# Kernel optimization log

Measured on AMD Instinct MI355X. Metric: run time of the kernel, lower is better.

Reference implementation:

```python
import jax, jax.numpy as jnp
import numpy as np

N_NODES = 50000
N_EDGES = 800000
VOCAB = 500
IN_DIM = 128
HID = 128
OUT_DIM = 64
N_GRAPHS = 512


def setup_inputs() -> dict:
    key = jax.random.key(0)
    ks = jax.random.split(key, 12)
    s = 0.05
    return {
        "emb": jax.random.normal(ks[0], (VOCAB, IN_DIM), jnp.float32) * s,
        "w1a": jax.random.normal(ks[1], (HID, IN_DIM), jnp.float32) * s,
        "b1a": jnp.zeros((HID,), jnp.float32),
        "w1b": jax.random.normal(ks[2], (HID, HID), jnp.float32) * s,
        "b1b": jnp.zeros((HID,), jnp.float32),
        "w2a": jax.random.normal(ks[3], (HID, HID), jnp.float32) * s,
        "b2a": jnp.zeros((HID,), jnp.float32),
        "w2b": jax.random.normal(ks[4], (HID, HID), jnp.float32) * s,
        "b2b": jnp.zeros((HID,), jnp.float32),
        "fc_w": jax.random.normal(ks[5], (OUT_DIM, HID), jnp.float32) * s,
        "fc_b": jnp.zeros((OUT_DIM,), jnp.float32),
        "x_idx": jax.random.randint(ks[6], (N_NODES,), 0, VOCAB, jnp.int32),
        "edge_index": jax.random.randint(ks[7], (2, N_EDGES), 0, N_NODES, jnp.int32),
        "batch": jnp.sort(jax.random.randint(ks[8], (N_NODES,), 0, N_GRAPHS, jnp.int32)),
    }


def gin_conv(x, wa, ba, wb, bb, src, dst):
    # GINConv with eps=0: MLP(x + sum_{j->i} x_j)
    agg = jax.ops.segment_sum(x[src], dst, num_segments=N_NODES)  # [N, d]
    h = x + agg
    h = jax.nn.relu(h @ wa.T + ba)
    return h @ wb.T + bb


def reference(emb, w1a, b1a, w1b, b1b, w2a, b2a, w2b, b2b, fc_w, fc_b,
              x_idx, edge_index, batch):
    src, dst = edge_index[0], edge_index[1]
    x = emb[x_idx]  # [N, IN_DIM] embedding lookup
    x = jax.nn.relu(gin_conv(x, w1a, b1a, w1b, b1b, src, dst))
    x = jax.nn.relu(gin_conv(x, w2a, b2a, w2b, b2b, src, dst))
    # global mean pool over graphs
    sums = jax.ops.segment_sum(x, batch, num_segments=N_GRAPHS)  # [G, HID]
    cnt = jax.ops.segment_sum(jnp.ones((N_NODES,), x.dtype), batch, num_segments=N_GRAPHS)
    pooled = sums / jnp.maximum(cnt, 1.0)[:, None]
    return pooled @ fc_w.T + fc_b  # [G, OUT_DIM]
```

## Files before the change

### kernel.cpp

```cpp
#include <hip/hip_runtime.h>

#define N_NODES 50000
#define N_EDGES 800000
#define DIM 128
#define NGRAPH 512
#define ODIM 64
#define VOCAB 500
#define NBKT 391
#define NB2 128
#define EPB2 (N_EDGES / NB2)
#define CAP 4096

typedef __attribute__((ext_vector_type(8))) short bf16x8;
typedef __attribute__((ext_vector_type(4))) short bf16x4;
typedef __attribute__((ext_vector_type(4))) float f32x4;

__device__ inline unsigned short f2bf(float f) {
  unsigned u = __builtin_bit_cast(unsigned, f);
  return (unsigned short)((u + 0x7fffu + ((u >> 16) & 1u)) >> 16);
}
__device__ inline float bf2f(unsigned short h) {
  unsigned u = ((unsigned)h) << 16;
  return __builtin_bit_cast(float, u);
}

__global__ __launch_bounds__(256) void prep_kernel(
    const float* __restrict__ emb,
    const float* __restrict__ w1a, const float* __restrict__ w1b,
    const float* __restrict__ w2a, const float* __restrict__ w2b,
    unsigned short* __restrict__ embb, unsigned short* __restrict__ wbf) {
  int u = blockIdx.x * 256 + threadIdx.x;
  const float* src;
  unsigned short* dst;
  if (u < VOCAB * 16) {
    src = emb + (size_t)u * 8;
    dst = embb + (size_t)u * 8;
  } else {
    int v = u - VOCAB * 16;
    if (v >= 4 * 2048) return;
    int m = v >> 11, loc = v & 2047;
    const float* w = (m == 0) ? w1a : (m == 1) ? w1b : (m == 2) ? w2a : w2b;
    src = w + (size_t)loc * 8;
    dst = wbf + (size_t)v * 8;
  }
  f32x4 a = ((const f32x4*)src)[0], b = ((const f32x4*)src)[1];
  bf16x8 o;
  #pragma unroll
  for (int e = 0; e < 4; ++e) {
    o[e] = (short)f2bf(a[e]);
    o[4 + e] = (short)f2bf(b[e]);
  }
  *(bf16x8*)dst = o;
}

__global__ __launch_bounds__(512) void bkt_hist_kernel(
    const int* __restrict__ ei, unsigned* __restrict__ HB) {
  __shared__ unsigned cnt[NBKT];
  int t = threadIdx.x, b = blockIdx.x;
  for (int i = t; i < NBKT; i += 512) cnt[i] = 0;
  __syncthreads();
  int base = b * EPB2;
  for (int i = t; i < EPB2; i += 512)
    atomicAdd(&cnt[(unsigned)ei[N_EDGES + base + i] >> 7], 1u);
  __syncthreads();
  for (int i = t; i < NBKT; i += 512) HB[(size_t)b * NBKT + i] = cnt[i];
}

__global__ __launch_bounds__(512) void bkt_scatter_kernel(
    const int* __restrict__ ei, const unsigned* __restrict__ HB,
    unsigned* __restrict__ eb, int* __restrict__ bktbase) {
  __shared__ unsigned cur[NBKT];
  __shared__ unsigned wsum[8];
  int t = threadIdx.x, b = blockIdx.x;
  int lane = t & 63, wid = t >> 6;
  unsigned pre = 0, tot = 0;
  if (t < NBKT) {
    for (int bb = 0; bb < NB2; ++bb) {
      unsigned h = HB[(size_t)bb * NBKT + t];
      pre += (bb < b) ? h : 0u;
      tot += h;
    }
  }
  unsigned s = tot;
  #pragma unroll
  for (int d = 1; d < 64; d <<= 1) {
    unsigned u = __shfl_up(s, d, 64);
    if (lane >= d) s += u;
  }
  if (lane == 63) wsum[wid] = s;
  __syncthreads();
  if (wid == 0) {
    unsigned ws = (lane < 8) ? wsum[lane] : 0u;
    #pragma unroll
    for (int d = 1; d < 8; d <<= 1) {
      unsigned u = __shfl_up(ws, d, 64);
      if (lane >= d) ws += u;
    }
    if (lane < 8) wsum[lane] = ws;
  }
  __syncthreads();
  unsigned base = s - tot + (wid ? wsum[wid - 1] : 0u);
  if (t < NBKT) cur[t] = base + pre;
  if (b == 0) {
    if (t < NBKT) bktbase[t] = (int)base;
    if (t == NBKT - 1) bktbase[NBKT] = (int)(base + tot);
  }
  __syncthreads();
  int ebase = b * EPB2;
  for (int i = t; i < EPB2; i += 512) {
    int sn = ei[ebase + i];
    unsigned d = (unsigned)ei[N_EDGES + ebase + i];
    unsigned pos = atomicAdd(&cur[d >> 7], 1u);
    eb[pos] = ((d & 127u) << 16) | (unsigned)sn;
  }
}

__global__ __launch_bounds__(512) void sort_bucket_kernel(
    const unsigned* __restrict__ eb, const int* __restrict__ bktbase,
    int* __restrict__ srt, int* __restrict__ row) {
  __shared__ unsigned stage[CAP];
  __shared__ unsigned short sorted[CAP];
  __shared__ unsigned hist[128], cur[128];
  __shared__ unsigned wtot;
  int t = threadIdx.x, bkt = blockIdx.x;
  int bs = bktbase[bkt], be = bktbase[bkt + 1];
  int cnt = be - bs;
  if (cnt > CAP) cnt = CAP;
  if (t < 128) hist[t] = 0;
  if (bkt == 0 && t == 0) row[N_NODES] = N_EDGES;
  __syncthreads();
  for (int i = t; i < cnt; i += 512) {
    unsigned e = eb[bs + i];
    stage[i] = e;
    atomicAdd(&hist[e >> 16], 1u);
  }
  __syncthreads();
  if (t < 128) {
    int lane = t & 63;
    unsigned v = hist[t], ss = v;
    #pragma unroll
    for (int d = 1; d < 64; d <<= 1) {
      unsigned u = __shfl_up(ss, d, 64);
      if (lane >= d) ss += u;
    }
    if (t == 63) wtot = ss;
    cur[t] = ss - v;
  }
  __syncthreads();
  if (t < 128) {
    unsigned e0 = cur[t] + (t >= 64 ? wtot : 0u);
    cur[t] = e0;
    int n = bkt * 128 + t;
    if (n < N_NODES) row[n] = bs + (int)e0;
  }
  __syncthreads();
  for (int i = t; i < cnt; i += 512) {
    unsigned e = stage[i];
    unsigned r = atomicAdd(&cur[e >> 16], 1u);
    sorted[r] = (unsigned short)(e & 0xFFFFu);
  }
  __syncthreads();
  for (int i = t; i < cnt; i += 512) srt[bs + i] = (int)sorted[i];
}

__global__ __launch_bounds__(256) void agg_emb_kernel(
    const unsigned short* __restrict__ embb, const int* __restrict__ xidx,
    const int* __restrict__ row, const int* __restrict__ srt,
    unsigned short* __restrict__ xa) {
  int n = blockIdx.x * 16 + (threadIdx.x >> 4);
  int c = threadIdx.x & 15;
  int lo = row[n], hi = row[n + 1];
  bf16x8 sv = *(const bf16x8*)(embb + (size_t)xidx[n] * DIM + c * 8);
  float a[8];
  #pragma unroll
  for (int e = 0; e < 8; ++e) a[e] = bf2f((unsigned short)sv[e]);
  int k = lo;
  for (; k + 8 <= hi; k += 8) {
    bf16x8 w[8];
    #pragma unroll
    for (int q = 0; q < 8; ++q)
      w[q] = *(const bf16x8*)(embb + (size_t)xidx[srt[k + q]] * DIM + c * 8);
    #pragma unroll
    for (int q = 0; q < 8; ++q)
      #pragma unroll
      for (int e = 0; e < 8; ++e) a[e] += bf2f((unsigned short)w[q][e]);
  }
  for (; k + 2 <= hi; k += 2) {
    bf16x8 w0 = *(const bf16x8*)(embb + (size_t)xidx[srt[k]] * DIM + c * 8);
    bf16x8 w1 = *(const bf16x8*)(embb + (size_t)xidx[srt[k + 1]] * DIM + c * 8);
    #pragma unroll
    for (int e = 0; e < 8; ++e)
      a[e] += bf2f((unsigned short)w0[e]) + bf2f((unsigned short)w1[e]);
  }
  if (k < hi) {
    bf16x8 w = *(const bf16x8*)(embb + (size_t)xidx[srt[k]] * DIM + c * 8);
    #pragma unroll
    for (int e = 0; e < 8; ++e) a[e] += bf2f((unsigned short)w[e]);
  }
  bf16x8 o;
  #pragma unroll
  for (int e = 0; e < 8; ++e) o[e] = (short)f2bf(a[e]);
  *(bf16x8*)(xa + (size_t)n * DIM + c * 8) = o;
}

__global__ __launch_bounds__(256) void agg_x_kernel(
    const unsigned short* __restrict__ x, const int* __restrict__ row,
    const int* __restrict__ srt, unsigned short* __restrict__ xa) {
  int n = blockIdx.x * 16 + (threadIdx.x >> 4);
  int c = threadIdx.x & 15;
  int lo = row[n], hi = row[n + 1];
  bf16x8 sv = *(const bf16x8*)(x + (size_t)n * DIM + c * 8);
  float a[8];
  #pragma unroll
  for (int e = 0; e < 8; ++e) a[e] = bf2f((unsigned short)sv[e]);
  int k = lo;
  for (; k + 8 <= hi; k += 8) {
    bf16x8 w[8];
    #pragma unroll
    for (int q = 0; q < 8; ++q)
      w[q] = *(const bf16x8*)(x + (size_t)srt[k + q] * DIM + c * 8);
    #pragma unroll
    for (int q = 0; q < 8; ++q)
      #pragma unroll
      for (int e = 0; e < 8; ++e) a[e] += bf2f((unsigned short)w[q][e]);
  }
  for (; k + 2 <= hi; k += 2) {
    bf16x8 w0 = *(const bf16x8*)(x + (size_t)srt[k] * DIM + c * 8);
    bf16x8 w1 = *(const bf16x8*)(x + (size_t)srt[k + 1] * DIM + c * 8);
    #pragma unroll
    for (int e = 0; e < 8; ++e)
      a[e] += bf2f((unsigned short)w0[e]) + bf2f((unsigned short)w1[e]);
  }
  if (k < hi) {
    bf16x8 w = *(const bf16x8*)(x + (size_t)srt[k] * DIM + c * 8);
    #pragma unroll
    for (int e = 0; e < 8; ++e) a[e] += bf2f((unsigned short)w[e]);
  }
  bf16x8 o;
  #pragma unroll
  for (int e = 0; e < 8; ++e) o[e] = (short)f2bf(a[e]);
  *(bf16x8*)(xa + (size_t)n * DIM + c * 8) = o;
}

__global__ __launch_bounds__(256) void mlp_mfma_kernel(
    const unsigned short* __restrict__ xa,
    const unsigned short* __restrict__ wabf, const float* __restrict__ ba,
    const unsigned short* __restrict__ wbbf, const float* __restrict__ bb,
    unsigned short* __restrict__ xout) {
  __shared__ short Xs[64 * 128];
  __shared__ short Hs[64 * 128];
  int t = threadIdx.x;
  int lane = t & 63;
  int w = t >> 6;
  int jq = w * 32;
  int l15 = lane & 15;
  int lg = lane >> 4;

  bf16x8 waf[2][4], wbf[2][4];
  #pragma unroll
  for (int jm = 0; jm < 2; ++jm) {
    int jrow = jq + jm * 16 + l15;
    #pragma unroll
    for (int ks = 0; ks < 4; ++ks) {
      int k0 = ks * 32 + lg * 8;
      waf[jm][ks] = *(const bf16x8*)(wabf + (size_t)jrow * DIM + k0);
      wbf[jm][ks] = *(const bf16x8*)(wbbf + (size_t)jrow * DIM + k0);
    }
  }
  f32x4 ba_r[2], bb_r[2];
  #pragma unroll
  for (int jm = 0; jm < 2; ++jm) {
    ba_r[jm] = *(const f32x4*)(ba + jq + jm * 16 + lg * 4);
    bb_r[jm] = *(const f32x4*)(bb + jq + jm * 16 + lg * 4);
  }

  for (int half = 0; half < 2; ++half) {
    int nbase = blockIdx.x * 128 + half * 64;

    {
      int r = t >> 2;
      int cb = (t & 3) * 4;
      int node = nbase + r;
      #pragma unroll
      for (int i = 0; i < 4; ++i) {
        int chunk = cb + i;
        bf16x8 v = {0, 0, 0, 0, 0, 0, 0, 0};
        if (node < N_NODES)
          v = *(const bf16x8*)(xa + (size_t)node * DIM + chunk * 8);
        *(bf16x8*)&Xs[r * 128 + ((chunk ^ (r & 7)) << 3)] = v;
      }
    }
    __syncthreads();

    #pragma unroll
    for (int nt = 0; nt < 4; ++nt) {
      int rrow = nt * 16 + l15;
      bf16x8 xf[4];
      #pragma unroll
      for (int ks = 0; ks < 4; ++ks) {
        int chunk = ks * 4 + lg;
        xf[ks] = *(const bf16x8*)&Xs[rrow * 128 + ((chunk ^ (rrow & 7)) << 3)];
      }
      #pragma unroll
      for (int jm = 0; jm < 2; ++jm) {
        f32x4 acc = ba_r[jm];
        #pragma unroll
        for (int ks = 0; ks < 4; ++ks)
          acc = __builtin_amdgcn_mfma_f32_16x16x32_bf16(waf[jm][ks], xf[ks], acc, 0, 0, 0);
        int hnode = nt * 16 + l15;
        int cbase = jq + jm * 16 + lg * 4;
        unsigned p0 = (unsigned)f2bf(fmaxf(acc[0], 0.f)) |
                      ((unsigned)f2bf(fmaxf(acc[1], 0.f)) << 16);
        unsigned p1 = (unsigned)f2bf(fmaxf(acc[2], 0.f)) |
                      ((unsigned)f2bf(fmaxf(acc[3], 0.f)) << 16);
        unsigned idx = hnode * 128 + (((cbase >> 3) ^ (hnode & 7)) << 3) + (cbase & 7);
        *(uint2*)&Hs[idx] = make_uint2(p0, p1);
      }
    }
    __syncthreads();

    #pragma unroll
    for (int nt = 0; nt < 4; ++nt) {
      int rrow = nt * 16 + l15;
      bf16x8 hf[4];
      #pragma unroll
      for (int ks = 0; ks < 4; ++ks) {
        int chunk = ks * 4 + lg;
        hf[ks] = *(const bf16x8*)&Hs[rrow * 128 + ((chunk ^ (rrow & 7)) << 3)];
      }
      #pragma unroll
      for (int jm = 0; jm < 2; ++jm) {
        f32x4 acc = bb_r[jm];
        #pragma unroll
        for (int ks = 0; ks < 4; ++ks)
          acc = __builtin_amdgcn_mfma_f32_16x16x32_bf16(wbf[jm][ks], hf[ks], acc, 0, 0, 0);
        int node = nbase + nt * 16 + l15;
        if (node < N_NODES) {
          bf16x4 o;
          #pragma unroll
          for (int e = 0; e < 4; ++e) o[e] = (short)f2bf(fmaxf(acc[e], 0.f));
          *(bf16x4*)(xout + (size_t)node * DIM + jq + jm * 16 + lg * 4) = o;
        }
      }
    }
    __syncthreads();
  }
}

#define PP 132
__global__ __launch_bounds__(256) void pool_fc_kernel(
    const unsigned short* __restrict__ x, const int* __restrict__ batch,
    const float* __restrict__ fcw, const float* __restrict__ fcb,
    float* __restrict__ out) {
  int g = blockIdx.x, t = threadIdx.x;
  __shared__ float part[16 * PP];
  __shared__ float pooled[DIM];
  __shared__ int sbound[2];
  if (t < 2) {
    int target = g + t;
    int lo = 0, hi = N_NODES;
    while (lo < hi) {
      int m = (lo + hi) >> 1;
      if (batch[m] < target) lo = m + 1; else hi = m;
    }
    sbound[t] = lo;
  }
  __syncthreads();
  int lo = sbound[0], hi = sbound[1];
  int r = t >> 4, c = t & 15;
  float acc[8] = {0.f, 0.f, 0.f, 0.f, 0.f, 0.f, 0.f, 0.f};
  for (int nn = lo + r; nn < hi; nn += 16) {
    bf16x8 v = *(const bf16x8*)(x + (size_t)nn * DIM + c * 8);
    #pragma unroll
    for (int e = 0; e < 8; ++e) acc[e] += bf2f((unsigned short)v[e]);
  }
  #pragma unroll
  for (int e = 0; e < 8; ++e) part[r * PP + c * 8 + e] = acc[e];
  __syncthreads();
  if (t < DIM) {
    float s = 0.f;
    #pragma unroll
    for (int rr = 0; rr < 16; ++rr) s += part[rr * PP + t];
    pooled[t] = s / fmaxf((float)(hi - lo), 1.0f);
  }
  __syncthreads();
  if (t < ODIM) {
    float a = fcb[t];
    const float* wr = fcw + (size_t)t * DIM;
    #pragma unroll 8
    for (int h = 0; h < DIM; ++h) a += pooled[h] * wr[h];
    out[(size_t)g * ODIM + t] = a;
  }
}

extern "C" void kernel_launch(void* const* d_in, const int* in_sizes, int n_in,
                              void* d_out, int out_size, void* d_ws, size_t ws_size,
                              hipStream_t stream) {
  const float* emb  = (const float*)d_in[0];
  const float* w1a  = (const float*)d_in[1];
  const float* b1a  = (const float*)d_in[2];
  const float* w1b  = (const float*)d_in[3];
  const float* b1b  = (const float*)d_in[4];
  const float* w2a  = (const float*)d_in[5];
  const float* b2a  = (const float*)d_in[6];
  const float* w2b  = (const float*)d_in[7];
  const float* b2b  = (const float*)d_in[8];
  const float* fcw  = (const float*)d_in[9];
  const float* fcb  = (const float*)d_in[10];
  const int*   xidx = (const int*)d_in[11];
  const int*   ei   = (const int*)d_in[12];
  const int*   batch= (const int*)d_in[13];
  float* out = (float*)d_out;

  size_t featb = (size_t)N_NODES * DIM * sizeof(unsigned short);
  char* ws = (char*)d_ws;
  unsigned short* B1 = (unsigned short*)ws;
  unsigned short* B2 = (unsigned short*)(ws + featb);
  char* p = ws + 2 * featb;
  unsigned short* embb = (unsigned short*)p;  p += (VOCAB * DIM * 2 + 15) / 16 * 16;
  unsigned short* wbf  = (unsigned short*)p;  p += (4 * DIM * DIM * 2 + 15) / 16 * 16;
  int* row  = (int*)p;      p += ((N_NODES + 1) * 4 + 15) / 16 * 16;
  int* bktbase = (int*)p;   p += ((NBKT + 1) * 4 + 15) / 16 * 16;
  unsigned* HB  = (unsigned*)p;  p += (size_t)NB2 * NBKT * 4;
  unsigned* eb  = (unsigned*)p;  p += (size_t)N_EDGES * 4;
  int* srt  = (int*)p;

  const unsigned short* w1abf = wbf;
  const unsigned short* w1bbf = wbf + DIM * DIM;
  const unsigned short* w2abf = wbf + 2 * DIM * DIM;
  const unsigned short* w2bbf = wbf + 3 * DIM * DIM;

  prep_kernel<<<(VOCAB * 16 + 4 * 2048 + 255) / 256, 256, 0, stream>>>(
      emb, w1a, w1b, w2a, w2b, embb, wbf);

  bkt_hist_kernel<<<NB2, 512, 0, stream>>>(ei, HB);
  bkt_scatter_kernel<<<NB2, 512, 0, stream>>>(ei, HB, eb, bktbase);
  sort_bucket_kernel<<<NBKT, 512, 0, stream>>>(eb, bktbase, srt, row);

  agg_emb_kernel<<<N_NODES / 16, 256, 0, stream>>>(embb, xidx, row, srt, B1);
  mlp_mfma_kernel<<<(N_NODES + 127) / 128, 256, 0, stream>>>(B1, w1abf, b1a, w1bbf, b1b, B2);

  agg_x_kernel<<<N_NODES / 16, 256, 0, stream>>>(B2, row, srt, B1);
  mlp_mfma_kernel<<<(N_NODES + 127) / 128, 256, 0, stream>>>(B1, w2abf, b2a, w2bbf, b2b, B2);

  pool_fc_kernel<<<NGRAPH, 256, 0, stream>>>(B2, batch, fcw, fcb, out);
}
```

Baseline: 128.1 us.

## Replace two-pass bucket scatter with fixed-capacity buckets and fuse sort with first aggregation

Swaps the histogram, global prefix-scan and scatter passes for a single build kernel. It reserves slots in fixed-capacity per-bucket regions using global atomics, with counters zeroed in the prep kernel. The per-bucket sort kernel now also does the first-layer embedding aggregation straight from its shared-memory sorted list. The edge index array is stored as 16-bit, and row bounds become separate lo and hi arrays. This removes two kernel launches and one global pass over the edges, but any edge beyond the per-bucket capacity is silently dropped, and the first aggregation now runs on only 391 blocks.

```diff
diff --git a/kernel.cpp b/kernel.cpp
--- a/kernel.cpp
+++ b/kernel.cpp
@@ -28,8 +28,10 @@
     const float* __restrict__ emb,
     const float* __restrict__ w1a, const float* __restrict__ w1b,
     const float* __restrict__ w2a, const float* __restrict__ w2b,
-    unsigned short* __restrict__ embb, unsigned short* __restrict__ wbf) {
+    unsigned short* __restrict__ embb, unsigned short* __restrict__ wbf,
+    int* __restrict__ gcnt) {
   int u = blockIdx.x * 256 + threadIdx.x;
+  if (u < NBKT) gcnt[u] = 0;
   const float* src;
   unsigned short* dst;
   if (u < VOCAB * 16) {
@@ -53,84 +55,51 @@
   *(bf16x8*)dst = o;
 }
 
-__global__ __launch_bounds__(512) void bkt_hist_kernel(
-    const int* __restrict__ ei, unsigned* __restrict__ HB) {
+__global__ __launch_bounds__(512) void build_kernel(
+    const int* __restrict__ ei, int* __restrict__ gcnt,
+    unsigned* __restrict__ eb) {
   __shared__ unsigned cnt[NBKT];
+  __shared__ unsigned base[NBKT];
   int t = threadIdx.x, b = blockIdx.x;
   for (int i = t; i < NBKT; i += 512) cnt[i] = 0;
   __syncthreads();
-  int base = b * EPB2;
+  int ebase = b * EPB2;
   for (int i = t; i < EPB2; i += 512)
-    atomicAdd(&cnt[(unsigned)ei[N_EDGES + base + i] >> 7], 1u);
-  __syncthreads();
-  for (int i = t; i < NBKT; i += 512) HB[(size_t)b * NBKT + i] = cnt[i];
-}
-
-__global__ __launch_bounds__(512) void bkt_scatter_kernel(
-    const int* __restrict__ ei, const unsigned* __restrict__ HB,
-    unsigned* __restrict__ eb, int* __restrict__ bktbase) {
-  __shared__ unsigned cur[NBKT];
-  __shared__ unsigned wsum[8];
-  int t = threadIdx.x, b = blockIdx.x;
-  int lane = t & 63, wid = t >> 6;
-  unsigned pre = 0, tot = 0;
-  if (t < NBKT) {
-    for (int bb = 0; bb < NB2; ++bb) {
-      unsigned h = HB[(size_t)bb * NBKT + t];
-      pre += (bb < b) ? h : 0u;
-      tot += h;
-    }
-  }
-  unsigned s = tot;
-  #pragma unroll
-  for (int d = 1; d < 64; d <<= 1) {
-    unsigned u = __shfl_up(s, d, 64);
-    if (lane >= d) s += u;
-  }
-  if (lane == 63) wsum[wid] = s;
-  __syncthreads();
-  if (wid == 0) {
-    unsigned ws = (lane < 8) ? wsum[lane] : 0u;
-    #pragma unroll
-    for (int d = 1; d < 8; d <<= 1) {
-      unsigned u = __shfl_up(ws, d, 64);
-      if (lane >= d) ws += u;
-    }
-    if (lane < 8) wsum[lane] = ws;
-  }
-  __syncthreads();
-  unsigned base = s - tot + (wid ? wsum[wid - 1] : 0u);
-  if (t < NBKT) cur[t] = base + pre;
-  if (b == 0) {
-    if (t < NBKT) bktbase[t] = (int)base;
-    if (t == NBKT - 1) bktbase[NBKT] = (int)(base + tot);
-  }
-  __syncthreads();
-  int ebase = b * EPB2;
+    atomicAdd(&cnt[(unsigned)ei[N_EDGES + ebase + i] >> 7], 1u);
+  __syncthreads();
+  for (int i = t; i < NBKT; i += 512) {
+    base[i] = (unsigned)atomicAdd(&gcnt[i], (int)cnt[i]);
+    cnt[i] = 0;
+  }
+  __syncthreads();
   for (int i = t; i < EPB2; i += 512) {
     int sn = ei[ebase + i];
     unsigned d = (unsigned)ei[N_EDGES + ebase + i];
-    unsigned pos = atomicAdd(&cur[d >> 7], 1u);
-    eb[pos] = ((d & 127u) << 16) | (unsigned)sn;
-  }
-}
-
-__global__ __launch_bounds__(512) void sort_bucket_kernel(
-    const unsigned* __restrict__ eb, const int* __restrict__ bktbase,
-    int* __restrict__ srt, int* __restrict__ row) {
+    unsigned bk = d >> 7;
+    unsigned r = atomicAdd(&cnt[bk], 1u);
+    unsigned pos = base[bk] + r;
+    if (pos < CAP)
+      eb[(size_t)bk * CAP + pos] = ((d & 127u) << 16) | (unsigned)sn;
+  }
+}
+
+__global__ __launch_bounds__(512) void sort_agg1_kernel(
+    const unsigned* __restrict__ eb, const int* __restrict__ gcnt,
+    const unsigned short* __restrict__ embb, const int* __restrict__ xidx,
+    unsigned short* __restrict__ srt16, int* __restrict__ rowlo,
+    int* __restrict__ rowhi, unsigned short* __restrict__ xa) {
   __shared__ unsigned stage[CAP];
   __shared__ unsigned short sorted[CAP];
   __shared__ unsigned hist[128], cur[128];
   __shared__ unsigned wtot;
   int t = threadIdx.x, bkt = blockIdx.x;
-  int bs = bktbase[bkt], be = bktbase[bkt + 1];
-  int cnt = be - bs;
+  int cnt = gcnt[bkt];
   if (cnt > CAP) cnt = CAP;
+  size_t ebbase = (size_t)bkt * CAP;
   if (t < 128) hist[t] = 0;
-  if (bkt == 0 && t == 0) row[N_NODES] = N_EDGES;
   __syncthreads();
   for (int i = t; i < cnt; i += 512) {
-    unsigned e = eb[bs + i];
+    unsigned e = eb[ebbase + i];
     stage[i] = e;
     atomicAdd(&hist[e >> 16], 1u);
   }
@@ -151,7 +120,10 @@
     unsigned e0 = cur[t] + (t >= 64 ? wtot : 0u);
     cur[t] = e0;
     int n = bkt * 128 + t;
-    if (n < N_NODES) row[n] = bs + (int)e0;
+    if (n < N_NODES) {
+      rowlo[n] = (int)(ebbase + e0);
+      rowhi[n] = (int)(ebbase + e0 + hist[t]);
+    }
   }
   __syncthreads();
   for (int i = t; i < cnt; i += 512) {
@@ -160,17 +132,58 @@
     sorted[r] = (unsigned short)(e & 0xFFFFu);
   }
   __syncthreads();
-  for (int i = t; i < cnt; i += 512) srt[bs + i] = (int)sorted[i];
-}
-
-__global__ __launch_bounds__(256) void agg_emb_kernel(
-    const unsigned short* __restrict__ embb, const int* __restrict__ xidx,
-    const int* __restrict__ row, const int* __restrict__ srt,
+
+  for (int i = t; i < cnt; i += 512) srt16[ebbase + i] = sorted[i];
+
+  int g = t >> 4, c = t & 15;
+  for (int ii = 0; ii < 4; ++ii) {
+    int dloc = ii * 32 + g;
+    int node = bkt * 128 + dloc;
+    if (node >= N_NODES) continue;
+    int hi = (int)cur[dloc];
+    int lo = hi - (int)hist[dloc];
+    bf16x8 sv = *(const bf16x8*)(embb + (size_t)xidx[node] * DIM + c * 8);
+    float a[8];
+    #pragma unroll
+    for (int e = 0; e < 8; ++e) a[e] = bf2f((unsigned short)sv[e]);
+    int k = lo;
+    for (; k + 8 <= hi; k += 8) {
+      bf16x8 w[8];
+      #pragma unroll
+      for (int q = 0; q < 8; ++q)
+        w[q] = *(const bf16x8*)(embb + (size_t)xidx[sorted[k + q]] * DIM + c * 8);
+      #pragma unroll
+      for (int q = 0; q < 8; ++q)
+        #pragma unroll
+        for (int e = 0; e < 8; ++e) a[e] += bf2f((unsigned short)w[q][e]);
+    }
+    for (; k + 2 <= hi; k += 2) {
+      bf16x8 w0 = *(const bf16x8*)(embb + (size_t)xidx[sorted[k]] * DIM + c * 8);
+      bf16x8 w1 = *(const bf16x8*)(embb + (size_t)xidx[sorted[k + 1]] * DIM + c * 8);
+      #pragma unroll
+      for (int e = 0; e < 8; ++e)
+        a[e] += bf2f((unsigned short)w0[e]) + bf2f((unsigned short)w1[e]);
+    }
+    if (k < hi) {
+      bf16x8 w = *(const bf16x8*)(embb + (size_t)xidx[sorted[k]] * DIM + c * 8);
+      #pragma unroll
+      for (int e = 0; e < 8; ++e) a[e] += bf2f((unsigned short)w[e]);
+    }
+    bf16x8 o;
+    #pragma unroll
+    for (int e = 0; e < 8; ++e) o[e] = (short)f2bf(a[e]);
+    *(bf16x8*)(xa + (size_t)node * DIM + c * 8) = o;
+  }
+}
+
+__global__ __launch_bounds__(256) void agg_x_kernel(
+    const unsigned short* __restrict__ x, const int* __restrict__ rowlo,
+    const int* __restrict__ rowhi, const unsigned short* __restrict__ srt16,
     unsigned short* __restrict__ xa) {
   int n = blockIdx.x * 16 + (threadIdx.x >> 4);
   int c = threadIdx.x & 15;
-  int lo = row[n], hi = row[n + 1];
-  bf16x8 sv = *(const bf16x8*)(embb + (size_t)xidx[n] * DIM + c * 8);
+  int lo = rowlo[n], hi = rowhi[n];
+  bf16x8 sv = *(const bf16x8*)(x + (size_t)n * DIM + c * 8);
   float a[8];
   #pragma unroll
   for (int e = 0; e < 8; ++e) a[e] = bf2f((unsigned short)sv[e]);
@@ -179,60 +192,21 @@
     bf16x8 w[8];
     #pragma unroll
     for (int q = 0; q < 8; ++q)
-      w[q] = *(const bf16x8*)(embb + (size_t)xidx[srt[k + q]] * DIM + c * 8);
+      w[q] = *(const bf16x8*)(x + (size_t)srt16[k + q] * DIM + c * 8);
     #pragma unroll
     for (int q = 0; q < 8; ++q)
       #pragma unroll
       for (int e = 0; e < 8; ++e) a[e] += bf2f((unsigned short)w[q][e]);
   }
   for (; k + 2 <= hi; k += 2) {
-    bf16x8 w0 = *(const bf16x8*)(embb + (size_t)xidx[srt[k]] * DIM + c * 8);
-    bf16x8 w1 = *(const bf16x8*)(embb + (size_t)xidx[srt[k + 1]] * DIM + c * 8);
+    bf16x8 w0 = *(const bf16x8*)(x + (size_t)srt16[k] * DIM + c * 8);
+    bf16x8 w1 = *(const bf16x8*)(x + (size_t)srt16[k + 1] * DIM + c * 8);
     #pragma unroll
     for (int e = 0; e < 8; ++e)
       a[e] += bf2f((unsigned short)w0[e]) + bf2f((unsigned short)w1[e]);
   }
   if (k < hi) {
-    bf16x8 w = *(const bf16x8*)(embb + (size_t)xidx[srt[k]] * DIM + c * 8);
-    #pragma unroll
-    for (int e = 0; e < 8; ++e) a[e] += bf2f((unsigned short)w[e]);
-  }
-  bf16x8 o;
-  #pragma unroll
-  for (int e = 0; e < 8; ++e) o[e] = (short)f2bf(a[e]);
-  *(bf16x8*)(xa + (size_t)n * DIM + c * 8) = o;
-}
-
-__global__ __launch_bounds__(256) void agg_x_kernel(
-    const unsigned short* __restrict__ x, const int* __restrict__ row,
-    const int* __restrict__ srt, unsigned short* __restrict__ xa) {
-  int n = blockIdx.x * 16 + (threadIdx.x >> 4);
-  int c = threadIdx.x & 15;
-  int lo = row[n], hi = row[n + 1];
-  bf16x8 sv = *(const bf16x8*)(x + (size_t)n * DIM + c * 8);
-  float a[8];
-  #pragma unroll
-  for (int e = 0; e < 8; ++e) a[e] = bf2f((unsigned short)sv[e]);
-  int k = lo;
-  for (; k + 8 <= hi; k += 8) {
-    bf16x8 w[8];
-    #pragma unroll
-    for (int q = 0; q < 8; ++q)
-      w[q] = *(const bf16x8*)(x + (size_t)srt[k + q] * DIM + c * 8);
-    #pragma unroll
-    for (int q = 0; q < 8; ++q)
-      #pragma unroll
-      for (int e = 0; e < 8; ++e) a[e] += bf2f((unsigned short)w[q][e]);
-  }
-  for (; k + 2 <= hi; k += 2) {
-    bf16x8 w0 = *(const bf16x8*)(x + (size_t)srt[k] * DIM + c * 8);
-    bf16x8 w1 = *(const bf16x8*)(x + (size_t)srt[k + 1] * DIM + c * 8);
-    #pragma unroll
-    for (int e = 0; e < 8; ++e)
-      a[e] += bf2f((unsigned short)w0[e]) + bf2f((unsigned short)w1[e]);
-  }
-  if (k < hi) {
-    bf16x8 w = *(const bf16x8*)(x + (size_t)srt[k] * DIM + c * 8);
+    bf16x8 w = *(const bf16x8*)(x + (size_t)srt16[k] * DIM + c * 8);
     #pragma unroll
     for (int e = 0; e < 8; ++e) a[e] += bf2f((unsigned short)w[e]);
   }
@@ -419,11 +393,11 @@
   char* p = ws + 2 * featb;
   unsigned short* embb = (unsigned short*)p;  p += (VOCAB * DIM * 2 + 15) / 16 * 16;
   unsigned short* wbf  = (unsigned short*)p;  p += (4 * DIM * DIM * 2 + 15) / 16 * 16;
-  int* row  = (int*)p;      p += ((N_NODES + 1) * 4 + 15) / 16 * 16;
-  int* bktbase = (int*)p;   p += ((NBKT + 1) * 4 + 15) / 16 * 16;
-  unsigned* HB  = (unsigned*)p;  p += (size_t)NB2 * NBKT * 4;
-  unsigned* eb  = (unsigned*)p;  p += (size_t)N_EDGES * 4;
-  int* srt  = (int*)p;
+  int* gcnt  = (int*)p;     p += (NBKT * 4 + 15) / 16 * 16;
+  int* rowlo = (int*)p;     p += ((size_t)N_NODES * 4 + 15) / 16 * 16;
+  int* rowhi = (int*)p;     p += ((size_t)N_NODES * 4 + 15) / 16 * 16;
+  unsigned* eb = (unsigned*)p;          p += (size_t)NBKT * CAP * 4;
+  unsigned short* srt16 = (unsigned short*)p;
 
   const unsigned short* w1abf = wbf;
   const unsigned short* w1bbf = wbf + DIM * DIM;
@@ -431,16 +405,14 @@
   const unsigned short* w2bbf = wbf + 3 * DIM * DIM;
 
   prep_kernel<<<(VOCAB * 16 + 4 * 2048 + 255) / 256, 256, 0, stream>>>(
-      emb, w1a, w1b, w2a, w2b, embb, wbf);
-
-  bkt_hist_kernel<<<NB2, 512, 0, stream>>>(ei, HB);
-  bkt_scatter_kernel<<<NB2, 512, 0, stream>>>(ei, HB, eb, bktbase);
-  sort_bucket_kernel<<<NBKT, 512, 0, stream>>>(eb, bktbase, srt, row);
-
-  agg_emb_kernel<<<N_NODES / 16, 256, 0, stream>>>(embb, xidx, row, srt, B1);
+      emb, w1a, w1b, w2a, w2b, embb, wbf, gcnt);
+
+  build_kernel<<<NB2, 512, 0, stream>>>(ei, gcnt, eb);
+
+  sort_agg1_kernel<<<NBKT, 512, 0, stream>>>(eb, gcnt, embb, xidx, srt16, rowlo, rowhi, B1);
   mlp_mfma_kernel<<<(N_NODES + 127) / 128, 256, 0, stream>>>(B1, w1abf, b1a, w1bbf, b1b, B2);
 
-  agg_x_kernel<<<N_NODES / 16, 256, 0, stream>>>(B2, row, srt, B1);
+  agg_x_kernel<<<N_NODES / 16, 256, 0, stream>>>(B2, rowlo, rowhi, srt16, B1);
   mlp_mfma_kernel<<<(N_NODES + 127) / 128, 256, 0, stream>>>(B1, w2abf, b2a, w2bbf, b2b, B2);
 
   pool_fc_kernel<<<NGRAPH, 256, 0, stream>>>(B2, batch, fcw, fcb, out);
```

Measured after the change: 120.6 us. -5.8%, faster.
